# Optimization experiments

Measured on AMD Instinct MI355X. Metric: run time of the kernel, lower is better.

The kernel has to match this reference:

```python
import jax, jax.numpy as jnp
import numpy as np

# STBLISModule forward. Original torch code materializes kron(s_wav, t_wav)
# [K*J, N*T, N*T] and contracts: filtered[b,c,d,nt] = sum_k kron[d,nt,k] x[b,c,k].
# Since kron(S_p, T_q)[n*T+t, m*T+u] = S_p[n,m] * T_q[t,u] (row-major flatten),
# this equals the separable form y[b,c,p,q] = S_p @ X[b,c] @ T_q^T, which we
# compute directly (identical math, no giant dense kron matrix).

B, C, N, T = 4, 4, 512, 256
K, J = 4, 4


def setup_inputs() -> dict:
    key = jax.random.key(0)
    k1, k2, k3 = jax.random.split(key, 3)
    x = jax.random.normal(k1, (B, C, N, T), dtype=jnp.float32)
    s_wav = jax.random.normal(k2, (K, N, N), dtype=jnp.float32)  # spatial wavelet bank
    t_wav = jax.random.normal(k3, (J, T, T), dtype=jnp.float32)  # temporal wavelet bank
    return {"x": x, "s_wav": s_wav, "t_wav": t_wav}


def reference(x, s_wav, t_wav):
    # spatial filtering: [B,C,K,N,T]
    tmp = jnp.einsum('pnm,bcmu->bcpnu', s_wav, x)
    # temporal filtering: [B,C,K,J,N,T]; note sum over last axis u of t_wav
    # matches kron/einsum 'ijk,mlk' contraction (i.e. X @ T_q^T)
    y = jnp.einsum('bcpnu,qtu->bcpqnt', tmp, t_wav)
    b, c, p, q, n, t = y.shape
    # D index ordering d = p*J + q matches torch.kron filter ordering
    y = y.reshape(b, c * p * q, n, t)
    # dual ReLU split, concatenated on channel dim
    return jnp.concatenate([jax.nn.relu(y), jax.nn.relu(-y)], axis=1)
```

## Files before the change

kernel.cpp:

```cpp
#include <hip/hip_runtime.h>
#include <hip/hip_bf16.h>

typedef __attribute__((ext_vector_type(8))) short bf16x8;
typedef __attribute__((ext_vector_type(4))) float f32x4;
typedef __attribute__((ext_vector_type(4))) int   i32x4;
typedef __attribute__((ext_vector_type(2))) int   i32x2;

#define DEV static __device__ __forceinline__

DEV unsigned short f2bf(float f) {
  __hip_bfloat16 h = __float2bfloat16(f);
  return __builtin_bit_cast(unsigned short, h);
}
DEV int pack2(float a, float b) {
  return (int)f2bf(a) | ((int)f2bf(b) << 16);
}
DEV bf16x8 ldsFrag(const char* lds, int off) {
  i32x4 v = *(const i32x4*)(lds + off);
  return __builtin_bit_cast(bf16x8, v);
}


__global__ __launch_bounds__(256) void cvt_all(
    const float* __restrict__ x, unsigned short* __restrict__ xt,
    const float* __restrict__ sw, unsigned short* __restrict__ swb,
    const float* __restrict__ tw, unsigned short* __restrict__ twb)
{
  const int bid = blockIdx.x;
  const int tid = threadIdx.x;
  if (bid < 512) {
    __shared__ unsigned short lt[64][72];
    const int ut = bid & 3;
    const int mt = (bid >> 2) & 7;
    const int bc = bid >> 5;
    const int ul = tid & 63;
    const int mr = tid >> 6;
    const float* px = x + ((size_t)bc * 512 + mt * 64) * 256 + ut * 64;
#pragma unroll
    for (int r = 0; r < 16; r++) {
      int m = r * 4 + mr;
      lt[m][ul] = f2bf(px[(size_t)m * 256 + ul]);
    }
    __syncthreads();
    const int t8 = tid >> 5;
    const int a  = t8 & 3;
    const int bb = t8 >> 2;
    const int l0 = tid & 31;
    unsigned short* tilep =
        xt + (((size_t)(bc * 16 + ut * 4 + a)) * 16 + (mt * 2 + bb)) * 512;
#pragma unroll
    for (int h = 0; h < 2; h++) {
      int l = l0 + h * 32;
      int ur = a * 16 + (l & 15);
      int mb = bb * 32 + (l >> 4) * 8;
      i32x4 w;
#pragma unroll
      for (int j = 0; j < 4; j++)
        w[j] = (int)lt[mb + 2 * j][ur] | ((int)lt[mb + 2 * j + 1][ur] << 16);
      *(i32x4*)(tilep + l * 8) = w;
    }
  } else if (bid < 1024) {
    const int tile = (bid - 512) * 4 + (tid >> 6);
    const int l = tid & 63;
    const int mt2 = tile & 15;
    const int nt2 = (tile >> 4) & 31;
    const int p   = tile >> 9;
    const float* ps = sw + ((size_t)p * 512 + nt2 * 16 + (l & 15)) * 512
                         + mt2 * 32 + (l >> 4) * 8;
    f32x4 A = ((const f32x4*)ps)[0], Bv = ((const f32x4*)ps)[1];
    i32x4 w;
    w[0] = pack2(A[0], A[1]);  w[1] = pack2(A[2], A[3]);
    w[2] = pack2(Bv[0], Bv[1]); w[3] = pack2(Bv[2], Bv[3]);
    *(i32x4*)(swb + (size_t)tile * 512 + l * 8) = w;
  } else {
    const int tile = (bid - 1024) * 4 + (tid >> 6);
    const int l = tid & 63;
    const int ut2 = tile & 7;
    const int tt2 = (tile >> 3) & 15;
    const int q   = tile >> 7;
    const float* pt = tw + ((size_t)q * 256 + tt2 * 16 + (l & 15)) * 256
                         + ut2 * 32 + (l >> 4) * 8;
    f32x4 A = ((const f32x4*)pt)[0], Bv = ((const f32x4*)pt)[1];
    i32x4 w;
    w[0] = pack2(A[0], A[1]);  w[1] = pack2(A[2], A[3]);
    w[2] = pack2(Bv[0], Bv[1]); w[3] = pack2(Bv[2], Bv[3]);
    *(i32x4*)(twb + (size_t)tile * 512 + l * 8) = w;
  }
}

__global__ __launch_bounds__(512, 4) void stblis_main(
    const unsigned short* __restrict__ xt, const unsigned short* __restrict__ swb,
    const unsigned short* __restrict__ twb, float* __restrict__ out)
{
  __shared__ __align__(16) char lds[32768];

  const int tid  = threadIdx.x;
  const int lane = tid & 63;
  const int wid  = tid >> 6;
  const int l15  = lane & 15;
  const int l4   = lane >> 4;

  const int bx = blockIdx.x;
  const int nt = bx & 7;
  const int p  = (bx >> 3) & 3;
  const int bc = bx >> 5;
  const int n0 = nt * 64;
  const int b = bc >> 2, c = bc & 3;

  const int wu = wid >> 1;
  const int wn = wid & 1;

  f32x4 acc[4][2];
#pragma unroll
  for (int i = 0; i < 4; i++)
#pragma unroll
    for (int j = 0; j < 2; j++) acc[i][j] = {0.f, 0.f, 0.f, 0.f};

  const unsigned short* xA = xt  + (((size_t)(bc * 16 + wu * 4)) * 16) * 512 + lane * 8;
  const unsigned short* sB = swb + (((size_t)(p * 32 + nt * 4 + wn * 2)) * 16) * 512 + lane * 8;

  for (int kc = 0; kc < 8; kc++) {
#pragma unroll
    for (int ks = 0; ks < 2; ks++) {
      const int mt2 = kc * 2 + ks;
      bf16x8 af[4], bg[2];
#pragma unroll
      for (int uf = 0; uf < 4; uf++)
        af[uf] = *(const bf16x8*)(xA + ((size_t)uf * 16 + mt2) * 512);
#pragma unroll
      for (int nf = 0; nf < 2; nf++)
        bg[nf] = *(const bf16x8*)(sB + ((size_t)nf * 16 + mt2) * 512);
#pragma unroll
      for (int uf = 0; uf < 4; uf++)
#pragma unroll
        for (int nf = 0; nf < 2; nf++)
          acc[uf][nf] = __builtin_amdgcn_mfma_f32_16x16x32_bf16(
              af[uf], bg[nf], acc[uf][nf], 0, 0, 0);
    }
  }

#pragma unroll
  for (int uf = 0; uf < 4; uf++)
#pragma unroll
    for (int nf = 0; nf < 2; nf++) {
      int u0 = wu * 64 + uf * 16 + l4 * 4;
      int n  = wn * 32 + nf * 16 + l15;
      i32x2 w;
      w[0] = pack2(acc[uf][nf][0], acc[uf][nf][1]);
      w[1] = pack2(acc[uf][nf][2], acc[uf][nf][3]);
      *(i32x2*)(lds + n * 512 + (((u0 >> 3) ^ (n & 7)) << 4) + (u0 & 7) * 2) = w;
    }
  __syncthreads();

  const int tq = wid >> 1;
  const int nh = wid & 1;

#define LOADBG(dst, ph)                                                        \
  {                                                                            \
    const int q_ = (ph) >> 2, tc_ = (ph) & 3;                                  \
    const unsigned short* tA_ =                                                \
        twb + (((size_t)(q_ * 16 + tc_ * 4 + tq)) * 8) * 512 + lane * 8;       \
    _Pragma("unroll")                                                          \
    for (int us = 0; us < 8; us++)                                             \
      dst[us] = *(const bf16x8*)(tA_ + (size_t)us * 512);                      \
  }

  bf16x8 bgA[8], bgB[8];
  LOADBG(bgA, 0);

  bf16x8 afr[8][2];
#pragma unroll
  for (int us = 0; us < 8; us++)
#pragma unroll
    for (int nf = 0; nf < 2; nf++) {
      int n = nh * 32 + nf * 16 + l15;
      afr[us][nf] = ldsFrag(lds, n * 512 + (((us * 4 + l4) ^ (n & 7)) << 4));
    }
  __syncthreads();

  char* const stg0 = lds;
  char* const stg1 = lds + 16384;

  auto body = [&](int ph, bf16x8 (&bg)[8], char* stgW) {
    const int q  = ph >> 2;
    const int tc = ph & 3;
    f32x4 a2[2];
    a2[0] = {0.f, 0.f, 0.f, 0.f};
    a2[1] = {0.f, 0.f, 0.f, 0.f};
#pragma unroll
    for (int us = 0; us < 8; us++) {
      a2[0] = __builtin_amdgcn_mfma_f32_16x16x32_bf16(bg[us], afr[us][0], a2[0], 0, 0, 0);
      a2[1] = __builtin_amdgcn_mfma_f32_16x16x32_bf16(bg[us], afr[us][1], a2[1], 0, 0, 0);
    }
#pragma unroll
    for (int nf = 0; nf < 2; nf++) {
      int n = nh * 32 + nf * 16 + l15;
      int c16 = tq * 4 + l4;
      *(f32x4*)(stgW + n * 256 + ((c16 ^ (n & 7)) << 4)) = a2[nf];
    }
    __syncthreads();
    float* outQP = out + ((size_t)(b * 128 + c * 16 + p * 4 + q) * 512 + n0) * 256;
    float* outQN = outQP + (size_t)64 * 512 * 256;
#pragma unroll
    for (int h = 0; h < 2; h++) {
      int cc  = tid + h * 512;
      int r   = cc >> 4;
      int o16 = cc & 15;
      f32x4 y = *(const f32x4*)(stgW + r * 256 + ((o16 ^ (r & 7)) << 4));
      f32x4 vP, vN;
#pragma unroll
      for (int j = 0; j < 4; j++) {
        vP[j] = fmaxf(y[j], 0.f);
        vN[j] = fmaxf(-y[j], 0.f);
      }
      size_t go = (size_t)r * 256 + tc * 64 + o16 * 4;
      *(f32x4*)(outQP + go) = vP;
      *(f32x4*)(outQN + go) = vN;
    }
  };

  for (int ph2 = 0; ph2 < 8; ph2++) {
    const int ph = ph2 * 2;
    LOADBG(bgB, ph + 1);
    body(ph, bgA, stg0);
    if (ph2 < 7) LOADBG(bgA, ph + 2);
    body(ph + 1, bgB, stg1);
  }
#undef LOADBG
}

extern "C" void kernel_launch(void* const* d_in, const int* in_sizes, int n_in,
                              void* d_out, int out_size, void* d_ws, size_t ws_size,
                              hipStream_t stream) {
  (void)in_sizes; (void)n_in; (void)out_size; (void)ws_size;
  const float* x  = (const float*)d_in[0];
  const float* sw = (const float*)d_in[1];
  const float* tw = (const float*)d_in[2];
  float* out = (float*)d_out;

  unsigned short* xt  = (unsigned short*)d_ws;
  unsigned short* swb = xt + (size_t)16 * 16 * 16 * 512;
  unsigned short* twb = swb + (size_t)2048 * 512;

  cvt_all<<<dim3(1152), dim3(256), 0, stream>>>(x, xt, sw, swb, tw, twb);
  stblis_main<<<dim3(512), dim3(512), 0, stream>>>(xt, swb, twb, out);
}
```

Baseline: 70.19 us.

## Stage full q-slab in 64KB LDS to cut barriers per output tile

The temporal stage now accumulates all four t-chunks of a given q into one 64KB LDS staging area, where it previously double-buffered one 64-wide chunk at a time. One barrier pair per q replaces one per chunk, and the epilogue writes full 256-float output rows with contiguous stores. The change doubles LDS use per block, which may lower occupancy from the requested 4 blocks per CU. It also drops the overlap that the double-buffered staging gave between MFMA work and global stores.

After: 143.2 us. 2.04x slower.

```diff
diff --git a/kernel.cpp b/kernel.cpp
--- a/kernel.cpp
+++ b/kernel.cpp
@@ -92,7 +92,7 @@
     const unsigned short* __restrict__ xt, const unsigned short* __restrict__ swb,
     const unsigned short* __restrict__ twb, float* __restrict__ out)
 {
-  __shared__ __align__(16) char lds[32768];
+  __shared__ __align__(16) char lds[65536];
 
   const int tid  = threadIdx.x;
   const int lane = tid & 63;
@@ -178,53 +178,57 @@
     }
   __syncthreads();
 
-  char* const stg0 = lds;
-  char* const stg1 = lds + 16384;
-
-  auto body = [&](int ph, bf16x8 (&bg)[8], char* stgW) {
-    const int q  = ph >> 2;
-    const int tc = ph & 3;
+  char* const stg = lds;
+
+  auto sub = [&](bf16x8 (&cur)[8], int tc) __attribute__((always_inline)) {
     f32x4 a2[2];
     a2[0] = {0.f, 0.f, 0.f, 0.f};
     a2[1] = {0.f, 0.f, 0.f, 0.f};
 #pragma unroll
     for (int us = 0; us < 8; us++) {
-      a2[0] = __builtin_amdgcn_mfma_f32_16x16x32_bf16(bg[us], afr[us][0], a2[0], 0, 0, 0);
-      a2[1] = __builtin_amdgcn_mfma_f32_16x16x32_bf16(bg[us], afr[us][1], a2[1], 0, 0, 0);
+      a2[0] = __builtin_amdgcn_mfma_f32_16x16x32_bf16(cur[us], afr[us][0], a2[0], 0, 0, 0);
+      a2[1] = __builtin_amdgcn_mfma_f32_16x16x32_bf16(cur[us], afr[us][1], a2[1], 0, 0, 0);
     }
 #pragma unroll
     for (int nf = 0; nf < 2; nf++) {
-      int n = nh * 32 + nf * 16 + l15;
-      int c16 = tq * 4 + l4;
-      *(f32x4*)(stgW + n * 256 + ((c16 ^ (n & 7)) << 4)) = a2[nf];
-    }
-    __syncthreads();
+      int n   = nh * 32 + nf * 16 + l15;
+      int c16 = tc * 16 + tq * 4 + l4;
+      *(f32x4*)(stg + n * 1024 + ((c16 ^ (n & 15)) << 4)) = a2[nf];
+    }
+  };
+
+  for (int q = 0; q < 4; q++) {
+    if (q) asm volatile("s_barrier" ::: "memory");
+
+#pragma unroll
+    for (int tch = 0; tch < 2; tch++) {
+      const int i0 = q * 4 + tch * 2;
+      LOADBG(bgB, i0 + 1);
+      sub(bgA, tch * 2);
+      if (i0 + 2 < 16) LOADBG(bgA, i0 + 2);
+      sub(bgB, tch * 2 + 1);
+    }
+
+    asm volatile("s_waitcnt lgkmcnt(0)\n\ts_barrier" ::: "memory");
+
     float* outQP = out + ((size_t)(b * 128 + c * 16 + p * 4 + q) * 512 + n0) * 256;
     float* outQN = outQP + (size_t)64 * 512 * 256;
 #pragma unroll
-    for (int h = 0; h < 2; h++) {
-      int cc  = tid + h * 512;
-      int r   = cc >> 4;
-      int o16 = cc & 15;
-      f32x4 y = *(const f32x4*)(stgW + r * 256 + ((o16 ^ (r & 7)) << 4));
+    for (int it = 0; it < 8; it++) {
+      int g   = it * 512 + tid;
+      int r   = g >> 6;
+      int c16 = g & 63;
+      f32x4 y = *(const f32x4*)(stg + r * 1024 + ((c16 ^ (r & 15)) << 4));
       f32x4 vP, vN;
 #pragma unroll
       for (int j = 0; j < 4; j++) {
         vP[j] = fmaxf(y[j], 0.f);
         vN[j] = fmaxf(-y[j], 0.f);
       }
-      size_t go = (size_t)r * 256 + tc * 64 + o16 * 4;
+      size_t go = (size_t)r * 256 + c16 * 4;
       *(f32x4*)(outQP + go) = vP;
       *(f32x4*)(outQN + go) = vN;
     }
-  };
-
-  for (int ph2 = 0; ph2 < 8; ph2++) {
-    const int ph = ph2 * 2;
-    LOADBG(bgB, ph + 1);
-    body(ph, bgA, stg0);
-    if (ph2 < 7) LOADBG(bgA, ph + 2);
-    body(ph + 1, bgB, stg1);
   }
 #undef LOADBG
 }
```
